# Kernel optimization log

Hardware: AMD Instinct MI355X
Metric: run time of the kernel (lower is better)

Reference implementation:

```python
import jax, jax.numpy as jnp
import numpy as np
from jax import lax

EPS = 1e-5

def conv2d(x, w, pad):
    # x: NCHW, w: OIHW
    return lax.conv_general_dilated(x, w, (1, 1), [(pad, pad), (pad, pad)],
                                    dimension_numbers=('NCHW', 'OIHW', 'NCHW'))

def batchnorm(x, gamma, beta):
    # training-mode BN: batch statistics over N,H,W (biased variance, as torch)
    m = jnp.mean(x, axis=(0, 2, 3), keepdims=True)
    v = jnp.var(x, axis=(0, 2, 3), keepdims=True)
    g = gamma.reshape(1, -1, 1, 1)
    b = beta.reshape(1, -1, 1, 1)
    return (x - m) * jax.lax.rsqrt(v + EPS) * g + b

def setup_inputs() -> dict:
    key = jax.random.key(0)
    ks = jax.random.split(key, 8)
    B, Cin, Cmid, NC, H, W = 4, 2048, 512, 19, 64, 64
    s = lambda fan: (2.0 / fan) ** 0.5
    return {
        'x':  jax.random.normal(ks[0], (B, Cin, H, W), jnp.float32),
        'Wa': jax.random.normal(ks[1], (Cmid, Cin, 3, 3), jnp.float32) * s(Cin * 9),
        'ga': jnp.ones((Cmid,), jnp.float32),
        'ba': jnp.zeros((Cmid,), jnp.float32),
        'Wb': jax.random.normal(ks[2], (Cmid, Cmid, 1, 1), jnp.float32) * s(Cmid),
        'bb': jnp.zeros((Cmid,), jnp.float32),
        'W1': jax.random.normal(ks[3], (Cmid, Cin + Cmid, 3, 3), jnp.float32) * s((Cin + Cmid) * 9),
        'g1': jnp.ones((Cmid,), jnp.float32),
        'b1': jnp.zeros((Cmid,), jnp.float32),
        'W4': jax.random.normal(ks[4], (NC, Cmid, 1, 1), jnp.float32) * s(Cmid),
        'b4': jnp.zeros((NC,), jnp.float32),
    }

def reference(x, Wa, ga, ba, Wb, bb, W1, g1, b1, W4, b4):
    # conva: 3x3 conv (no bias) -> BN -> ReLU
    out = jax.nn.relu(batchnorm(conv2d(x, Wa, 1), ga, ba))
    # convb: 1x1 conv with bias
    out = conv2d(out, Wb, 0) + bb.reshape(1, -1, 1, 1)
    # concat input with projected features along channels
    out = jnp.concatenate([x, out], axis=1)  # [B, Cin+Cmid, H, W]
    # b1 (3x3, no bias) -> b2 BN -> b3 ReLU
    out = jax.nn.relu(batchnorm(conv2d(out, W1, 1), g1, b1))
    # b4: 1x1 classifier conv with bias
    out_final = conv2d(out, W4, 0) + b4.reshape(1, -1, 1, 1)
    return (out, out_final)
```

## Files before the change

### kernel.cpp

```cpp
#include <hip/hip_runtime.h>

typedef unsigned short ushort_t;
typedef unsigned int uint_t;
typedef unsigned long long ulong_t;

typedef __bf16 bf16x8 __attribute__((ext_vector_type(8)));
typedef float f32x4 __attribute__((ext_vector_type(4)));
typedef float f32x16 __attribute__((ext_vector_type(16)));
typedef unsigned short u16x4 __attribute__((ext_vector_type(4)));

#define DEV __device__ __forceinline__
#define SB() __builtin_amdgcn_sched_barrier(0)
#define WAITV(n) asm volatile("s_waitcnt vmcnt(" #n ")" ::: "memory")

DEV ushort_t f2bf(float x) {
  uint_t u = __float_as_uint(x);
  u += 0x7fffu + ((u >> 16) & 1u);
  return (ushort_t)(u >> 16);
}
DEV float bf2f(ushort_t h) { return __uint_as_float(((uint_t)h) << 16); }

DEV void gload16(ulong_t g, const void* l) {
  __builtin_amdgcn_global_load_lds(
      (__attribute__((address_space(1))) void*)g,
      (__attribute__((address_space(3))) void*)(void*)l,
      16, 0, 0);
}
DEV int nxt3(int x) { return x == 2 ? 0 : x + 1; }

__global__ void zero_k(float* __restrict__ p, int n) {
  int i = blockIdx.x * 256 + threadIdx.x;
  if (i < n) p[i] = 0.f;
}

__global__ __launch_bounds__(256) void cvt_x_k(const float* __restrict__ X,
                                               ushort_t* __restrict__ P) {
  __shared__ float T[64][65];
  const int t = threadIdx.x;
  const int p0 = blockIdx.x * 64;
  const int c0 = blockIdx.y * 64;
  const int b = p0 >> 12;
  const int pin0 = p0 & 4095;
#pragma unroll
  for (int it = 0; it < 4; ++it) {
    const int cl = it * 16 + (t >> 4);
    const int pl = (t & 15) * 4;
    const f32x4 v = *(const f32x4*)&X[((size_t)(b * 2048 + c0 + cl)) * 4096 + pin0 + pl];
#pragma unroll
    for (int j = 0; j < 4; ++j) T[cl][pl + j] = v[j];
  }
  __syncthreads();
#pragma unroll
  for (int it = 0; it < 4; ++it) {
    const int pl = it * 16 + (t >> 4);
    const int cl = (t & 15) * 4;
    u16x4 h, l;
#pragma unroll
    for (int j = 0; j < 4; ++j) {
      float v = T[cl + j][pl];
      ushort_t hh = f2bf(v);
      h[j] = hh;
      l[j] = f2bf(v - bf2f(hh));
    }
    const int c = c0 + cl;
    const size_t o = (size_t)(p0 + pl) * 4096 + (size_t)((c >> 5) << 6) + (c & 31);
    *(u16x4*)&P[o] = h;
    *(u16x4*)&P[o + 32] = l;
  }
}

__global__ __launch_bounds__(256) void cvt_w3_k(const float* __restrict__ W,
                                                ushort_t* __restrict__ P,
                                                int I, int O) {
  const int t = threadIdx.x;
  const int o = blockIdx.y;
  const int i = blockIdx.x * 256 + t;
  const float* src = W + ((size_t)o * I + i) * 9;
  float v[9];
#pragma unroll
  for (int j = 0; j < 9; ++j) v[j] = src[j];
#pragma unroll
  for (int j = 0; j < 9; ++j) {
    ushort_t h = f2bf(v[j]);
    const size_t d = (size_t)(j * O + o) * (I * 2) + (size_t)((i >> 5) << 6) + (i & 31);
    P[d] = h;
    P[d + 32] = f2bf(v[j] - bf2f(h));
  }
}

__global__ __launch_bounds__(256) void cvt_e_k(const float* __restrict__ W,
                                               ushort_t* __restrict__ P) {
  int i = blockIdx.x * 256 + threadIdx.x;
  float v = W[i];
  ushort_t h = f2bf(v);
  const int o = i >> 9, ic = i & 511;
  const size_t d = (size_t)o * 1024 + (size_t)((ic >> 5) << 6) + (ic & 31);
  P[d] = h;
  P[d + 32] = f2bf(v - bf2f(h));
}

__global__ __launch_bounds__(256) void stats_k(const float* __restrict__ X,
                                               float* __restrict__ S,
                                               float* __restrict__ Q) {
  const int t = threadIdx.x;
  const int r0 = blockIdx.x * 32;
  const int c = t * 2;
  float s0 = 0, s1 = 0, q0 = 0, q1 = 0;
  for (int r = 0; r < 32; ++r) {
    const float2 v = *(const float2*)&X[((size_t)(r0 + r)) * 512 + c];
    s0 += v.x; s1 += v.y;
    q0 += v.x * v.x; q1 += v.y * v.y;
  }
  atomicAdd(&S[c], s0); atomicAdd(&S[c + 1], s1);
  atomicAdd(&Q[c], q0); atomicAdd(&Q[c + 1], q1);
}

__global__ void bnparams_k(const float* __restrict__ S, const float* __restrict__ Q,
                           const float* __restrict__ g, const float* __restrict__ b,
                           float* __restrict__ sc, float* __restrict__ sh) {
  const int t = threadIdx.x;
  const float m = S[t] * (1.0f / 16384.0f);
  const float v = Q[t] * (1.0f / 16384.0f) - m * m;
  const float inv = rsqrtf(v + 1e-5f);
  const float s = g[t] * inv;
  sc[t] = s;
  sh[t] = b[t] - m * s;
}

__global__ __launch_bounds__(256) void bnact_k(const float* __restrict__ X,
                                               const float* __restrict__ sc,
                                               const float* __restrict__ sh,
                                               ushort_t* __restrict__ P) {
  const size_t i0 = ((size_t)blockIdx.x * 256 + threadIdx.x) * 16;
  const int c0 = (int)(i0 & 511);
  const size_t px = i0 >> 9;
#pragma unroll
  for (int q = 0; q < 4; ++q) {
    const f32x4 v = *(const f32x4*)&X[i0 + q * 4];
    const f32x4 s = *(const f32x4*)&sc[c0 + q * 4];
    const f32x4 d = *(const f32x4*)&sh[c0 + q * 4];
    u16x4 h, l;
#pragma unroll
    for (int j = 0; j < 4; ++j) {
      float y = fmaf(v[j], s[j], d[j]);
      y = fmaxf(y, 0.f);
      ushort_t hh = f2bf(y);
      h[j] = hh;
      l[j] = f2bf(y - bf2f(hh));
    }
    const int c = c0 + q * 4;
    const size_t o = px * 1024 + (size_t)((c >> 5) << 6) + (c & 31);
    *(u16x4*)&P[o] = h;
    *(u16x4*)&P[o + 32] = l;
  }
}

__global__ __launch_bounds__(256) void bn_nchw_k(const float* __restrict__ X,
                                                 const float* __restrict__ sc,
                                                 const float* __restrict__ sh,
                                                 float* __restrict__ O) {
  __shared__ float T[64][65];
  const int t = threadIdx.x;
  const int p0 = blockIdx.x * 64;
  const int c0 = blockIdx.y * 64;
  const int b = p0 >> 12, pin0 = p0 & 4095;
#pragma unroll
  for (int it = 0; it < 4; ++it) {
    const int pl = it * 16 + (t >> 4);
    const int cl = (t & 15) * 4;
    const f32x4 v = *(const f32x4*)&X[((size_t)(p0 + pl)) * 512 + c0 + cl];
#pragma unroll
    for (int j = 0; j < 4; ++j) {
      float y = fmaf(v[j], sc[c0 + cl + j], sh[c0 + cl + j]);
      T[pl][cl + j] = fmaxf(y, 0.f);
    }
  }
  __syncthreads();
#pragma unroll
  for (int it = 0; it < 4; ++it) {
    const int cl = it * 16 + (t >> 4);
    const int pl = (t & 15) * 4;
    f32x4 o;
#pragma unroll
    for (int j = 0; j < 4; ++j) o[j] = T[pl + j][cl];
    *(f32x4*)&O[((size_t)(b * 512 + c0 + cl)) * 4096 + pin0 + pl] = o;
  }
}

__global__ __launch_bounds__(256) void conv4_k(const float* __restrict__ X,
                                               const float* __restrict__ sc,
                                               const float* __restrict__ sh,
                                               const float* __restrict__ W4,
                                               const float* __restrict__ B4,
                                               float* __restrict__ O) {
  __shared__ float A[256][69];
  __shared__ float WL[64][19];
  const int t = threadIdx.x;
  const int g0 = blockIdx.x * 256;
  float acc[19];
#pragma unroll
  for (int n = 0; n < 19; ++n) acc[n] = 0.f;
  for (int kc = 0; kc < 8; ++kc) {
    const int k0 = kc * 64;
    __syncthreads();
#pragma unroll
    for (int it = 0; it < 16; ++it) {
      const int rl = it * 16 + (t >> 4);
      const int cl = (t & 15) * 4;
      const f32x4 v = *(const f32x4*)&X[((size_t)(g0 + rl)) * 512 + k0 + cl];
#pragma unroll
      for (int j = 0; j < 4; ++j)
        A[rl][cl + j] = fmaxf(fmaf(v[j], sc[k0 + cl + j], sh[k0 + cl + j]), 0.f);
    }
    for (int e = t; e < 1216; e += 256) {
      int k = e / 19, n = e - k * 19;
      WL[k][n] = W4[(size_t)n * 512 + k0 + k];
    }
    __syncthreads();
#pragma unroll 8
    for (int k = 0; k < 64; ++k) {
      const float a = A[t][k];
#pragma unroll
      for (int n = 0; n < 19; ++n) acc[n] = fmaf(a, WL[k][n], acc[n]);
    }
  }
  const int g = g0 + t;
  const int b = g >> 12, pin = g & 4095;
#pragma unroll
  for (int n = 0; n < 19; ++n)
    O[((size_t)(b * 19 + n)) * 4096 + pin] = acc[n] + B4[n];
}

template <int TAPS, int EPI>
__global__ __launch_bounds__(512, 2) void conv_k(
    const ushort_t* __restrict__ A1, int S1, int CB1,
    const ushort_t* __restrict__ A2, int S2, int CB2,
    const ushort_t* __restrict__ WB, int CBt,
    const ushort_t* __restrict__ zp,
    float* __restrict__ Co, ushort_t* __restrict__ Cp,
    const float* __restrict__ bias) {
  constexpr int RW = (TAPS == 9) ? 6 : 4;
  constexpr int PB = RW * 2;
  constexpr int SPD = PB * 2;
  constexpr int AI = (2 * SPD) / 8;
  constexpr int APL = SPD * 1024;
  constexpr int ABUF = 2 * APL;
  __shared__ char lds_all[163840];
  char* Ald = lds_all;
  char* Bld = lds_all + 98304;
  const int t = threadIdx.x, lane = t & 63, wid = t >> 6;
  const int wr = wid >> 1, wc = wid & 1;
  const int gid = blockIdx.x, xcd = gid & 7, k_ = gid >> 3;
  const int by = xcd * 8 + (k_ & 7), bx = k_ >> 3;
  const int b = by >> 4, r0 = (by & 15) * 4, bbase = b * 4096;
  const int pxl = lane & 31;
  const int khalf = lane >> 5;
  const int lofs = lane * 16;
  const int NBS = CBt * 64;

  auto stageA = [&](int cb, int bufA) {
#pragma unroll
    for (int i = 0; i < AI; ++i) {
      const int g = wid * AI + i;
      const int d = g / SPD, rem = g - d * SPD;
      const int pxb = rem >> 1, kk = rem & 1;
      const int p = pxb * 32 + pxl;
      const int irow = r0 + (p >> 6) - ((TAPS == 9) ? 1 : 0);
      int cbl = cb;
      const ushort_t* base = A1;
      int S = S1;
      if (CB2 > 0 && cbl >= CB1) { base = A2; S = S2; cbl -= CB1; }
      const int gpx = bbase + irow * 64 + (p & 63);
      const ulong_t el = (ulong_t)gpx * (uint_t)S +
                         (uint_t)(cbl * 64 + d * 32 + (kk * 2 + khalf) * 8);
      const bool oob = (unsigned)irow >= 64u;
      const ulong_t src = oob ? (ulong_t)(zp + lane * 8) : (ulong_t)(base + el);
      gload16(src, Ald + bufA + d * APL + (pxb * 2 + kk) * 1024);
    }
  };
  auto stageB = [&](int cb, int tapIdx, int bufB) {
#pragma unroll
    for (int q = 0; q < 2; ++q) {
      const int s = wid * 2 + q;
      const int d = s >> 3, rem = s & 7, cob = rem >> 1, kk = rem & 1;
      const int co = bx * 128 + cob * 32 + pxl;
      const ulong_t el = (ulong_t)(tapIdx * 512 + co) * (uint_t)NBS +
                         (uint_t)(cb * 64 + d * 32 + (kk * 2 + khalf) * 8);
      gload16((ulong_t)(WB + el), Bld + bufB + d * 8192 + (cob * 2 + kk) * 1024);
    }
  };

  f32x16 acc[2][2];
#pragma unroll
  for (int i = 0; i < 2; ++i)
#pragma unroll
    for (int j2 = 0; j2 < 2; ++j2) acc[i][j2] = (f32x16){0.f};

  auto compute = [&](int abufB, int bbufB, int prow, int dx) {
    const char* Ab = Ald + abufB;
    const char* Bb = Bld + bbufB;
    bf16x8 a[2][2][2], bf[2][2][2];
#pragma unroll
    for (int ni = 0; ni < 2; ++ni)
#pragma unroll
      for (int kk = 0; kk < 2; ++kk) {
        const int bo = (wc * 2 + ni) * 2048 + kk * 1024 + lofs;
        bf[ni][kk][0] = *(const bf16x8*)(Bb + bo);
        bf[ni][kk][1] = *(const bf16x8*)(Bb + 8192 + bo);
      }
#pragma unroll
    for (int mi = 0; mi < 2; ++mi) {
      const int pb0 = prow * 2 + mi;
      int ao0;
      if (dx == 0) {
        ao0 = pb0 * 2048 + lofs;
      } else {
        int px = pb0 * 32 + pxl + dx;
        px = px < 0 ? 0 : (px > RW * 64 - 1 ? RW * 64 - 1 : px);
        ao0 = (px >> 5) * 2048 + khalf * 512 + (px & 31) * 16;
      }
#pragma unroll
      for (int kk = 0; kk < 2; ++kk) {
        const int ao = ao0 + kk * 1024;
        a[mi][kk][0] = *(const bf16x8*)(Ab + ao);
        a[mi][kk][1] = *(const bf16x8*)(Ab + APL + ao);
      }
    }
    if (TAPS == 9) {
      if (dx == -1 && pxl == 0) {
        bf16x8 z = {};
        a[0][0][0] = z; a[0][0][1] = z; a[0][1][0] = z; a[0][1][1] = z;
      }
      if (dx == 1 && pxl == 31) {
        bf16x8 z = {};
        a[1][0][0] = z; a[1][0][1] = z; a[1][1][0] = z; a[1][1][1] = z;
      }
    }
#pragma unroll
    for (int kk = 0; kk < 2; ++kk) {
#pragma unroll
      for (int mi = 0; mi < 2; ++mi)
#pragma unroll
        for (int ni = 0; ni < 2; ++ni)
          acc[mi][ni] = __builtin_amdgcn_mfma_f32_32x32x16_bf16(
              a[mi][kk][0], bf[ni][kk][0], acc[mi][ni], 0, 0, 0);
#pragma unroll
      for (int mi = 0; mi < 2; ++mi)
#pragma unroll
        for (int ni = 0; ni < 2; ++ni)
          acc[mi][ni] = __builtin_amdgcn_mfma_f32_32x32x16_bf16(
              a[mi][kk][0], bf[ni][kk][1], acc[mi][ni], 0, 0, 0);
#pragma unroll
      for (int mi = 0; mi < 2; ++mi)
#pragma unroll
        for (int ni = 0; ni < 2; ++ni)
          acc[mi][ni] = __builtin_amdgcn_mfma_f32_32x32x16_bf16(
              a[mi][kk][1], bf[ni][kk][0], acc[mi][ni], 0, 0, 0);
    }
  };

  if constexpr (TAPS == 9) {
    const int NT = CBt * 9;
    stageA(0, 0);
    stageB(0, 0, 0);
    stageB(0, 1, 16384);
    for (int T = 0; T < NT; T += 2) {
      SB();
      WAITV(0);
      SB();
      __builtin_amdgcn_s_barrier();
      SB();
      const int T2 = T + 2, T3 = T + 3;
      if (T2 < NT) {
        const int cs2 = T2 / 9, tp2 = T2 - cs2 * 9;
        if (tp2 == 0) stageA(cs2, (cs2 & 1) * ABUF);
        stageB(cs2, tp2, (T2 & 3) * 16384);
      }
      if (T3 < NT) {
        const int cs3 = T3 / 9, tp3 = T3 - cs3 * 9;
        if (tp3 == 0) stageA(cs3, (cs3 & 1) * ABUF);
        stageB(cs3, tp3, (T3 & 3) * 16384);
      }
      {
        const int cs = T / 9, tap = T - cs * 9;
        compute((cs & 1) * ABUF, (T & 3) * 16384, wr + tap / 3, tap % 3 - 1);
      }
      {
        const int T1 = T + 1;
        const int cs = T1 / 9, tap = T1 - cs * 9;
        compute((cs & 1) * ABUF, (T1 & 3) * 16384, wr + tap / 3, tap % 3 - 1);
      }
    }
  } else {
    int rr = 0;
    stageA(0, 0);
    stageB(0, 0, 0);
    SB();
    stageA(1, ABUF);
    stageB(1, 0, 16384);
    for (int cs = 0; cs < CBt; ++cs) {
      SB();
      WAITV(6);
      SB();
      __builtin_amdgcn_s_barrier();
      SB();
      const int rr2 = nxt3(nxt3(rr));
      stageA(cs + 2, rr2 * ABUF);
      stageB(cs + 2, 0, rr2 * 16384);
      compute(rr * ABUF, rr * 16384, wr, 0);
      rr = nxt3(rr);
    }
  }

  const int row0 = by * 256 + wr * 64;
  const int col0 = bx * 128 + wc * 64;
  const int rb = 4 * khalf;
  if (EPI == 0) {
#pragma unroll
    for (int mi = 0; mi < 2; ++mi)
#pragma unroll
      for (int ni = 0; ni < 2; ++ni) {
        const int c = col0 + ni * 32 + pxl;
#pragma unroll
        for (int rg = 0; rg < 16; ++rg) {
          const int r = row0 + mi * 32 + (rg & 3) + 8 * (rg >> 2) + rb;
          Co[(size_t)r * 512 + c] = acc[mi][ni][rg];
        }
      }
  } else {
#pragma unroll
    for (int ni = 0; ni < 2; ++ni) {
      const int c = col0 + ni * 32 + pxl;
      const float bv = bias[c];
      const size_t cg = (size_t)((c >> 5) << 6) + (c & 31);
#pragma unroll
      for (int mi = 0; mi < 2; ++mi)
#pragma unroll
        for (int rg = 0; rg < 16; ++rg) {
          const int r = row0 + mi * 32 + (rg & 3) + 8 * (rg >> 2) + rb;
          const float v = acc[mi][ni][rg] + bv;
          const ushort_t h = f2bf(v);
          Cp[(size_t)r * 1024 + cg] = h;
          Cp[(size_t)r * 1024 + cg + 32] = f2bf(v - bf2f(h));
        }
    }
  }
}

extern "C" void kernel_launch(void* const* d_in, const int* in_sizes, int n_in,
                              void* d_out, int out_size, void* d_ws, size_t ws_size,
                              hipStream_t stream) {
  const float* x  = (const float*)d_in[0];
  const float* Wa = (const float*)d_in[1];
  const float* ga = (const float*)d_in[2];
  const float* ba = (const float*)d_in[3];
  const float* Wb = (const float*)d_in[4];
  const float* bb = (const float*)d_in[5];
  const float* W1 = (const float*)d_in[6];
  const float* g1 = (const float*)d_in[7];
  const float* b1 = (const float*)d_in[8];
  const float* W4 = (const float*)d_in[9];
  const float* b4 = (const float*)d_in[10];
  float* out0 = (float*)d_out;
  float* outF = out0 + (size_t)4 * 512 * 64 * 64;

  char* ws = (char*)d_ws;
  size_t off = 0;
  auto take = [&](size_t bytes) -> char* {
    char* p = ws + off;
    off += (bytes + 255) & ~(size_t)255;
    return p;
  };
  const size_t PAD = 16384;
  ushort_t* zp  = (ushort_t*)take(8192);
  float* sumA = (float*)take(2048);
  float* ssA  = (float*)take(2048);
  float* scA  = (float*)take(2048);
  float* shA  = (float*)take(2048);
  float* sum1 = (float*)take(2048);
  float* ss1  = (float*)take(2048);
  float* sc1  = (float*)take(2048);
  float* sh1  = (float*)take(2048);
  ushort_t* X2  = (ushort_t*)take((size_t)16384 * 4096 * 2 + PAD);
  ushort_t* WA2 = (ushort_t*)take((size_t)9 * 512 * 4096 * 2 + PAD);
  ushort_t* W12 = (ushort_t*)take((size_t)9 * 512 * 5120 * 2 + PAD);
  ushort_t* WBb = (ushort_t*)take((size_t)512 * 1024 * 2 + PAD);
  ushort_t* oA2 = (ushort_t*)take((size_t)16384 * 1024 * 2 + PAD);
  ushort_t* oB2 = (ushort_t*)take((size_t)16384 * 1024 * 2 + PAD);
  float* convaRaw = (float*)take((size_t)16384 * 512 * 4);
  float* conv1Raw = (float*)take((size_t)16384 * 512 * 4);
  if (ws_size < off) return;

  zero_k<<<dim3(24), dim3(256), 0, stream>>>((float*)ws, 6144);
  cvt_x_k<<<dim3(256, 32), dim3(256), 0, stream>>>(x, X2);
  cvt_w3_k<<<dim3(8, 512), dim3(256), 0, stream>>>(Wa, WA2, 2048, 512);
  cvt_w3_k<<<dim3(10, 512), dim3(256), 0, stream>>>(W1, W12, 2560, 512);
  cvt_e_k<<<dim3(1024), dim3(256), 0, stream>>>(Wb, WBb);

  conv_k<9, 0><<<dim3(256), dim3(512), 0, stream>>>(
      X2, 4096, 64, X2, 4096, 0, WA2, 64, zp, convaRaw, nullptr, nullptr);
  stats_k<<<dim3(512), dim3(256), 0, stream>>>(convaRaw, sumA, ssA);
  bnparams_k<<<dim3(1), dim3(512), 0, stream>>>(sumA, ssA, ga, ba, scA, shA);
  bnact_k<<<dim3(2048), dim3(256), 0, stream>>>(convaRaw, scA, shA, oA2);

  conv_k<1, 1><<<dim3(256), dim3(512), 0, stream>>>(
      oA2, 1024, 18, oA2, 1024, 0, WBb, 16, zp, nullptr, oB2, bb);

  conv_k<9, 0><<<dim3(256), dim3(512), 0, stream>>>(
      X2, 4096, 64, oB2, 1024, 16, W12, 80, zp, conv1Raw, nullptr, nullptr);
  stats_k<<<dim3(512), dim3(256), 0, stream>>>(conv1Raw, sum1, ss1);
  bnparams_k<<<dim3(1), dim3(512), 0, stream>>>(sum1, ss1, g1, b1, sc1, sh1);

  bn_nchw_k<<<dim3(256, 8), dim3(256), 0, stream>>>(conv1Raw, sc1, sh1, out0);
  conv4_k<<<dim3(64), dim3(256), 0, stream>>>(conv1Raw, sc1, sh1, W4, b4, outF);
}
```

Before: 2.015 ms.

## Split conv1 into x-part and oB-part, accumulating into partial result

The second 3x3 conv over the concatenated input is split in two. The x-channel portion (64 channel blocks) now runs right after conva, since it does not depend on the conva/convb chain. A later pass over only the 16 oB2 channel blocks loads the partial fp32 result as its initial accumulator. This reorders work but adds an extra fp32 read and write of conv1Raw, plus a second kernel's prologue and epilogue. Kernels on one stream still serialize, so any gain would have to come from lower dependency or tail cost rather than real overlap.

```diff
diff --git a/kernel.cpp b/kernel.cpp
--- a/kernel.cpp
+++ b/kernel.cpp
@@ -231,11 +231,11 @@
     O[((size_t)(b * 19 + n)) * 4096 + pin] = acc[n] + B4[n];
 }
 
-template <int TAPS, int EPI>
+template <int TAPS, int EPI, int AINIT>
 __global__ __launch_bounds__(512, 2) void conv_k(
     const ushort_t* __restrict__ A1, int S1, int CB1,
     const ushort_t* __restrict__ A2, int S2, int CB2,
-    const ushort_t* __restrict__ WB, int CBt,
+    const ushort_t* __restrict__ WB, int CBt, int NBS, int cbOff,
     const ushort_t* __restrict__ zp,
     float* __restrict__ Co, ushort_t* __restrict__ Cp,
     const float* __restrict__ bias) {
@@ -256,7 +256,9 @@
   const int pxl = lane & 31;
   const int khalf = lane >> 5;
   const int lofs = lane * 16;
-  const int NBS = CBt * 64;
+  const int row0 = by * 256 + wr * 64;
+  const int col0 = bx * 128 + wc * 64;
+  const int rb = 4 * khalf;
 
   auto stageA = [&](int cb, int bufA) {
 #pragma unroll
@@ -285,16 +287,30 @@
       const int d = s >> 3, rem = s & 7, cob = rem >> 1, kk = rem & 1;
       const int co = bx * 128 + cob * 32 + pxl;
       const ulong_t el = (ulong_t)(tapIdx * 512 + co) * (uint_t)NBS +
-                         (uint_t)(cb * 64 + d * 32 + (kk * 2 + khalf) * 8);
+                         (uint_t)((cb + cbOff) * 64 + d * 32 + (kk * 2 + khalf) * 8);
       gload16((ulong_t)(WB + el), Bld + bufB + d * 8192 + (cob * 2 + kk) * 1024);
     }
   };
 
   f32x16 acc[2][2];
-#pragma unroll
-  for (int i = 0; i < 2; ++i)
-#pragma unroll
-    for (int j2 = 0; j2 < 2; ++j2) acc[i][j2] = (f32x16){0.f};
+  if constexpr (AINIT) {
+#pragma unroll
+    for (int mi = 0; mi < 2; ++mi)
+#pragma unroll
+      for (int ni = 0; ni < 2; ++ni) {
+        const int c = col0 + ni * 32 + pxl;
+#pragma unroll
+        for (int rg = 0; rg < 16; ++rg) {
+          const int r = row0 + mi * 32 + (rg & 3) + 8 * (rg >> 2) + rb;
+          acc[mi][ni][rg] = Co[(size_t)r * 512 + c];
+        }
+      }
+  } else {
+#pragma unroll
+    for (int i = 0; i < 2; ++i)
+#pragma unroll
+      for (int j2 = 0; j2 < 2; ++j2) acc[i][j2] = (f32x16){0.f};
+  }
 
   auto compute = [&](int abufB, int bbufB, int prow, int dx) {
     const char* Ab = Ald + abufB;
@@ -412,9 +428,6 @@
     }
   }
 
-  const int row0 = by * 256 + wr * 64;
-  const int col0 = bx * 128 + wc * 64;
-  const int rb = 4 * khalf;
   if (EPI == 0) {
 #pragma unroll
     for (int mi = 0; mi < 2; ++mi)
@@ -497,17 +510,22 @@
   cvt_w3_k<<<dim3(10, 512), dim3(256), 0, stream>>>(W1, W12, 2560, 512);
   cvt_e_k<<<dim3(1024), dim3(256), 0, stream>>>(Wb, WBb);
 
-  conv_k<9, 0><<<dim3(256), dim3(512), 0, stream>>>(
-      X2, 4096, 64, X2, 4096, 0, WA2, 64, zp, convaRaw, nullptr, nullptr);
+  conv_k<9, 0, 0><<<dim3(256), dim3(512), 0, stream>>>(
+      X2, 4096, 64, X2, 4096, 0, WA2, 64, 4096, 0, zp, convaRaw, nullptr, nullptr);
+
+  conv_k<9, 0, 0><<<dim3(256), dim3(512), 0, stream>>>(
+      X2, 4096, 64, X2, 4096, 0, W12, 64, 5120, 0, zp, conv1Raw, nullptr, nullptr);
+
   stats_k<<<dim3(512), dim3(256), 0, stream>>>(convaRaw, sumA, ssA);
   bnparams_k<<<dim3(1), dim3(512), 0, stream>>>(sumA, ssA, ga, ba, scA, shA);
   bnact_k<<<dim3(2048), dim3(256), 0, stream>>>(convaRaw, scA, shA, oA2);
 
-  conv_k<1, 1><<<dim3(256), dim3(512), 0, stream>>>(
-      oA2, 1024, 18, oA2, 1024, 0, WBb, 16, zp, nullptr, oB2, bb);
-
-  conv_k<9, 0><<<dim3(256), dim3(512), 0, stream>>>(
-      X2, 4096, 64, oB2, 1024, 16, W12, 80, zp, conv1Raw, nullptr, nullptr);
+  conv_k<1, 1, 0><<<dim3(256), dim3(512), 0, stream>>>(
+      oA2, 1024, 18, oA2, 1024, 0, WBb, 16, 1024, 0, zp, nullptr, oB2, bb);
+
+  conv_k<9, 0, 1><<<dim3(256), dim3(512), 0, stream>>>(
+      oB2, 1024, 16, oB2, 1024, 0, W12, 16, 5120, 64, zp, conv1Raw, nullptr, nullptr);
+
   stats_k<<<dim3(512), dim3(256), 0, stream>>>(conv1Raw, sum1, ss1);
   bnparams_k<<<dim3(1), dim3(512), 0, stream>>>(sum1, ss1, g1, b1, sc1, sh1);
 
```

New measurement: 2.032 ms. No clear change (+0.8%).
